# Optimization experiments

Hardware: AMD Instinct MI355X
Metric: run time of the kernel (lower is better)

The kernel has to match this reference:

```python
import jax, jax.numpy as jnp
import numpy as np


def silu(x):
    return x * jax.nn.sigmoid(x)


def conv1x1(x, w, s, b, act):
    # x: [B,Ci,H,W], w: [Co,Ci]; BN folded into per-channel scale s / bias b
    y = jnp.einsum('oi,bihw->bohw', w, x) * s[None, :, None, None] + b[None, :, None, None]
    return silu(y) if act else y


def dwconv3x3(x, w, s, b):
    # depthwise 3x3, groups=C, padding SAME (autopad=1); w: [C,1,3,3]
    y = jax.lax.conv_general_dilated(
        x, w, window_strides=(1, 1), padding=[(1, 1), (1, 1)],
        dimension_numbers=('NCHW', 'OIHW', 'NCHW'),
        feature_group_count=x.shape[1])
    return y * s[None, :, None, None] + b[None, :, None, None]


def attention(x, qkv_w, qkv_s, qkv_b, pe_w, pe_s, pe_b, proj_w, proj_s, proj_b,
              num_heads=4, key_dim=32, head_dim=64):
    B, C, H, W = x.shape
    N = H * W
    scale = key_dim ** -0.5
    qkv = conv1x1(x, qkv_w, qkv_s, qkv_b, act=False)          # [B, C+2*nh*kd, H, W]
    qkv = qkv.reshape(B, num_heads, key_dim * 2 + head_dim, N)
    q = qkv[:, :, :key_dim]                                    # [B,nh,kd,N]
    k = qkv[:, :, key_dim:2 * key_dim]                         # [B,nh,kd,N]
    v = qkv[:, :, 2 * key_dim:]                                # [B,nh,hd,N]
    attn = jnp.einsum('bhdi,bhdj->bhij', q, k) * scale         # [B,nh,N,N]
    attn = jax.nn.softmax(attn, axis=-1)
    out = jnp.einsum('bhdj,bhij->bhdi', v, attn)               # [B,nh,hd,N]
    out = out.reshape(B, C, H, W) + dwconv3x3(v.reshape(B, C, H, W), pe_w, pe_s, pe_b)
    return conv1x1(out, proj_w, proj_s, proj_b, act=False)


def setup_inputs() -> dict:
    key = jax.random.key(0)
    ks = jax.random.split(key, 32)
    B, C1, H, W = 4, 512, 48, 48
    c = C1 // 2  # 256
    h = c + 2 * 32 * 4  # 512
    d = {'x': jax.random.normal(ks[0], (B, C1, H, W), jnp.float32)}
    def w(i, shape):
        return jax.random.normal(ks[i], shape, jnp.float32) * 0.05
    def s(i, n):
        return jax.random.uniform(ks[i], (n,), jnp.float32, 0.5, 1.5)
    def b(i, n):
        return jax.random.normal(ks[i], (n,), jnp.float32) * 0.05
    d['cv1_w'], d['cv1_s'], d['cv1_b'] = w(1, (2 * c, C1)), s(2, 2 * c), b(3, 2 * c)
    d['qkv_w'], d['qkv_s'], d['qkv_b'] = w(4, (h, c)), s(5, h), b(6, h)
    d['pe_w'], d['pe_s'], d['pe_b'] = w(7, (c, 1, 3, 3)), s(8, c), b(9, c)
    d['proj_w'], d['proj_s'], d['proj_b'] = w(10, (c, c)), s(11, c), b(12, c)
    d['ffn1_w'], d['ffn1_s'], d['ffn1_b'] = w(13, (2 * c, c)), s(14, 2 * c), b(15, 2 * c)
    d['ffn2_w'], d['ffn2_s'], d['ffn2_b'] = w(16, (c, 2 * c)), s(17, c), b(18, c)
    d['cv2_w'], d['cv2_s'], d['cv2_b'] = w(19, (C1, 2 * c)), s(20, C1), b(21, C1)
    return d


def reference(x, cv1_w, cv1_s, cv1_b, qkv_w, qkv_s, qkv_b, pe_w, pe_s, pe_b,
              proj_w, proj_s, proj_b, ffn1_w, ffn1_s, ffn1_b, ffn2_w, ffn2_s, ffn2_b,
              cv2_w, cv2_s, cv2_b):
    c = cv1_w.shape[0] // 2  # hidden channels (256)
    ab = conv1x1(x, cv1_w, cv1_s, cv1_b, act=True)
    a, bb = ab[:, :c], ab[:, c:]
    bb = bb + attention(bb, qkv_w, qkv_s, qkv_b, pe_w, pe_s, pe_b,
                        proj_w, proj_s, proj_b)
    f = conv1x1(bb, ffn1_w, ffn1_s, ffn1_b, act=True)
    bb = bb + conv1x1(f, ffn2_w, ffn2_s, ffn2_b, act=False)
    return conv1x1(jnp.concatenate([a, bb], axis=1), cv2_w, cv2_s, cv2_b, act=True)
```

## Files before the change

kernel.cpp:

```cpp
#include <hip/hip_runtime.h>
#include <math.h>

#define N_SP 2304
#define HW 48

typedef unsigned short u16;
typedef short s8v  __attribute__((ext_vector_type(8)));
typedef short s4v  __attribute__((ext_vector_type(4)));
typedef u16   u16x8 __attribute__((ext_vector_type(8)));
typedef float f32x4 __attribute__((ext_vector_type(4)));
typedef unsigned u32x4 __attribute__((ext_vector_type(4)));

__device__ __forceinline__ short f2bf(float x) {
    unsigned u = __float_as_uint(x);
    u += 0x7FFFu + ((u >> 16) & 1u);
    return (short)(u >> 16);
}
__device__ __forceinline__ float bf2f(u16 u) {
    return __uint_as_float((unsigned)u << 16);
}
__device__ __forceinline__ float fexp2(float x) { return __builtin_amdgcn_exp2f(x); }
__device__ __forceinline__ float frcp(float x)  { return __builtin_amdgcn_rcpf(x); }
__device__ __forceinline__ float fsilu(float v) {
    return v * frcp(1.f + fexp2(-1.4426950408889634f * v));
}
__device__ __forceinline__ unsigned cvtpk(float lo, float hi) {
    unsigned r;
    asm("v_cvt_pk_bf16_f32 %0, %1, %2" : "=v"(r) : "v"(lo), "v"(hi));
    return r;
}
__device__ __forceinline__ void gload16(const void* g, void* l) {
    __builtin_amdgcn_global_load_lds(
        (const __attribute__((address_space(1))) void*)g,
        (__attribute__((address_space(3))) void*)l, 16, 0, 0);
}
__device__ __forceinline__ void bar_lgkm() {
    asm volatile("s_waitcnt lgkmcnt(0)" ::: "memory");
    __builtin_amdgcn_s_barrier();
}

__global__ __launch_bounds__(256) void prep(
    const float* __restrict__ X, u16* __restrict__ XT,
    const float* __restrict__ s0, const float* __restrict__ s1,
    const float* __restrict__ s2, const float* __restrict__ s3,
    const float* __restrict__ s4, const float* __restrict__ s5,
    u16* __restrict__ d0, u16* __restrict__ d1, u16* __restrict__ d2,
    u16* __restrict__ d3, u16* __restrict__ d4, u16* __restrict__ d5)
{
    __shared__ float tile[64][65];
    const int t = threadIdx.x;
    if (blockIdx.x < 960) {
        int id = blockIdx.x * 256 + t;
        const int c0 = 65536, c1 = c0 + 32768, c2 = c1 + 16384,
                  c3 = c2 + 32768, c4 = c3 + 32768, c5 = c4 + 65536;
        if (id >= c5) return;
        const float* s; u16* d; int off;
        if      (id < c0) { s = s0; d = d0; off = id; }
        else if (id < c1) { s = s1; d = d1; off = id - c0; }
        else if (id < c2) { s = s2; d = d2; off = id - c1; }
        else if (id < c3) { s = s3; d = d3; off = id - c2; }
        else if (id < c4) { s = s4; d = d4; off = id - c3; }
        else              { s = s5; d = d5; off = id - c4; }
        float4 v = ((const float4*)s)[off];
        s4v p; p[0] = f2bf(v.x); p[1] = f2bf(v.y); p[2] = f2bf(v.z); p[3] = f2bf(v.w);
        ((s4v*)d)[off] = p;
        return;
    }
    const int bid = blockIdx.x - 960;
    const int n0 = (bid % 36) * 64, c0 = ((bid / 36) & 7) * 64, b = bid / 288;
    const float* src = X + (long)b * 512 * N_SP;
    u16* dst = XT + (long)b * N_SP * 512;
    #pragma unroll
    for (int it = 0; it < 16; ++it) {
        int id = t + 256 * it;
        int cl = id >> 6, nl = id & 63;
        tile[cl][nl] = src[(long)(c0 + cl) * N_SP + n0 + nl];
    }
    __syncthreads();
    #pragma unroll
    for (int it = 0; it < 16; ++it) {
        int id = t + 256 * it;
        int nl = id >> 6, cl = id & 63;
        dst[(long)(n0 + nl) * 512 + c0 + cl] = f2bf(tile[cl][nl]);
    }
}

template <int NO, int OMODE>
__global__ __launch_bounds__(256) void mfma_gemm(
    const u16* __restrict__ A1, const u16* __restrict__ A2, int K1,
    int sA1, int sA2, int K,
    const u16* __restrict__ W,
    const float* __restrict__ S, const float* __restrict__ Bi,
    const u16* __restrict__ Res, int sR,
    void* __restrict__ OutP, u16* __restrict__ OutT, int sO, int Mtot,
    int act)
{
    __shared__ u16 Al[3][64][64];
    __shared__ u16 Bl[3][64][64];
    const int t  = threadIdx.x;
    const int p = blockIdx.x;
    const int cx = p & 7, q = p >> 3;
    const int n0 = (cx * 18 + q / NO) * 64;
    const int o0 = (q % NO) * 64;
    const int lane = t & 63, w = t >> 6;
    const int wn = (w & 1) * 32, wo = (w >> 1) * 32;
    const int li = lane & 15, g = lane >> 4;

    const int b_blk = n0 / N_SP;
    const int n_in0 = n0 - b_blk * N_SP;

    f32x4 acc[2][2];
    #pragma unroll
    for (int fm = 0; fm < 2; ++fm)
        #pragma unroll
        for (int fn = 0; fn < 2; ++fn) acc[fm][fn] = f32x4{0.f, 0.f, 0.f, 0.f};

    auto issue = [&](int buf, int k0) {
        #pragma unroll
        for (int qq = 0; qq < 2; ++qq) {
            int c = t + qq * 256;
            int row = c >> 3;
            int col = ((c & 7) ^ (row & 7)) * 8;
            int kk = k0 + col;
            const u16* ga = (kk < K1) ? (A1 + (long)(n0 + row) * sA1 + kk)
                                      : (A2 + (long)(n0 + row) * sA2 + (kk - K1));
            gload16(ga, (u16*)Al[buf] + (qq * 256 + w * 64) * 8);
            gload16(W + (long)(o0 + row) * K + k0 + col,
                    (u16*)Bl[buf] + (qq * 256 + w * 64) * 8);
        }
    };

    const int NK = K >> 6;
    issue(0, 0);
    if (NK > 1) issue(1, 64);

    for (int ks = 0; ks < NK; ++ks) {
        if (ks + 1 < NK) asm volatile("s_waitcnt vmcnt(4)" ::: "memory");
        else             asm volatile("s_waitcnt vmcnt(0)" ::: "memory");
        __builtin_amdgcn_s_barrier();
        if (ks + 2 < NK) issue((ks + 2) % 3, (ks + 2) << 6);
        const int cur = ks % 3;
        #pragma unroll
        for (int k2 = 0; k2 < 2; ++k2) {
            s8v af[2], bfv[2];
            #pragma unroll
            for (int fm = 0; fm < 2; ++fm) {
                int row = wn + fm * 16 + li;
                af[fm] = *(const s8v*)&Al[cur][row][((g + 4 * k2) ^ (li & 7)) * 8];
            }
            #pragma unroll
            for (int fn = 0; fn < 2; ++fn) {
                int row = wo + fn * 16 + li;
                bfv[fn] = *(const s8v*)&Bl[cur][row][((g + 4 * k2) ^ (li & 7)) * 8];
            }
            #pragma unroll
            for (int fm = 0; fm < 2; ++fm)
                #pragma unroll
                for (int fn = 0; fn < 2; ++fn)
                    acc[fm][fn] = __builtin_amdgcn_mfma_f32_16x16x32_bf16(
                        af[fm], bfv[fn], acc[fm][fn], 0, 0, 0);
        }
    }

    #pragma unroll
    for (int fn = 0; fn < 2; ++fn) {
        const int o = o0 + wo + fn * 16 + li;
        const float sc2 = S[o], bi = Bi[o];
        #pragma unroll
        for (int fm = 0; fm < 2; ++fm) {
            const int nb  = n0 + wn + fm * 16 + 4 * g;
            const int nib = n_in0 + wn + fm * 16 + 4 * g;
            float y[4];
            #pragma unroll
            for (int r = 0; r < 4; ++r) {
                float v = acc[fm][fn][r] * sc2 + bi;
                if (act) v = fsilu(v);
                y[r] = v;
            }
            if (Res) {
                #pragma unroll
                for (int r = 0; r < 4; ++r)
                    y[r] += bf2f(Res[(long)(nb + r) * sR + o]);
            }
            if (OMODE == 0) {
                u16* O = (u16*)OutP;
                #pragma unroll
                for (int r = 0; r < 4; ++r)
                    O[(long)(nb + r) * sO + o] = (u16)f2bf(y[r]);
            } else if (OMODE == 1 || OMODE == 3) {
                u16* O = (u16*)OutP + (long)b_blk * Mtot * N_SP + (long)o * N_SP + nib;
                s4v pk;
                #pragma unroll
                for (int r = 0; r < 4; ++r) pk[r] = f2bf(y[r]);
                *(s4v*)O = pk;
                if (OMODE == 3) {
                    #pragma unroll
                    for (int r = 0; r < 4; ++r)
                        OutT[(long)(nb + r) * 512 + o] = (u16)f2bf(y[r]);
                }
            } else {
                float* O = (float*)OutP + (long)b_blk * Mtot * N_SP + (long)o * N_SP + nib;
                *(float4*)O = make_float4(y[0], y[1], y[2], y[3]);
            }
        }
    }
}

__global__ __launch_bounds__(256) void attn_mfma(const u16* __restrict__ qkv,
    const u16* __restrict__ qkvT,
    u16* __restrict__ Opart, float* __restrict__ mpart, float* __restrict__ lpart)
{
    const int N = N_SP;
    __shared__ u16 Klds[2][64][40];
    __shared__ u16 Vlds[2][64][72];

    const int p = blockIdx.x;
    const int cx = p & 7, q = p >> 3;
    const int i0 = (q % 18) * 128;
    const int bhz = cx + 8 * (q / 18);
    const int bh = bhz & 15, z = bhz >> 4;
    const int b = bh >> 2, h = bh & 3;
    const int t = threadIdx.x;
    const int w = t >> 6;
    const int lane = t & 63;
    const int li = lane & 15;
    const int g  = lane >> 4;
    const float qscale = 0.17677669529663687f * 1.4426950408889634f;

    const u16* qp  = qkv  + ((long)b * 512 + (long)h * 128) * N;
    const u16* vp  = qp + 64L * N;
    const u16* qTp = qkvT + (long)b * N * 512 + h * 128;

    const int ia = i0 + w * 16 + li;
    const int ib = ia + 64;

    s8v qf[2];
    {
        s8v qa = *(const s8v*)(qTp + (long)ia * 512 + 8 * g);
        s8v qb = *(const s8v*)(qTp + (long)ib * 512 + 8 * g);
        #pragma unroll
        for (int r = 0; r < 8; ++r) {
            qf[0][r] = f2bf(bf2f((u16)qa[r]) * qscale);
            qf[1][r] = f2bf(bf2f((u16)qb[r]) * qscale);
        }
    }

    f32x4 oacc[2][4];
    #pragma unroll
    for (int q2 = 0; q2 < 2; ++q2)
        #pragma unroll
        for (int dt = 0; dt < 4; ++dt) oacc[q2][dt] = f32x4{0.f, 0.f, 0.f, 0.f};
    float m_run[2] = {-1e30f, -1e30f}, l_run[2] = {0.f, 0.f};

    const int kj2 = t & 63;
    const int kd  = (t >> 6) * 8;
    const int vd  = t >> 2;
    const int vjb = (t & 3) * 16;

    const int jbase = z * 576;
    u16x8 kr, vr0, vr1;
    auto ldregs = [&](int j0) {
        kr  = *(const u16x8*)(qTp + (long)(j0 + kj2) * 512 + 32 + kd);
        vr0 = *(const u16x8*)(vp + (long)vd * N + j0 + vjb);
        vr1 = *(const u16x8*)(vp + (long)vd * N + j0 + vjb + 8);
    };

    ldregs(jbase);
    *(u16x8*)&Klds[0][kj2][kd]     = kr;
    *(u16x8*)&Vlds[0][vd][vjb]     = vr0;
    *(u16x8*)&Vlds[0][vd][vjb + 8] = vr1;
    ldregs(jbase + 64);
    bar_lgkm();

    int cur = 0;
    for (int it = 0; it < 9; ++it) {
        if (it + 1 < 9) {
            *(u16x8*)&Klds[cur ^ 1][kj2][kd]     = kr;
            *(u16x8*)&Vlds[cur ^ 1][vd][vjb]     = vr0;
            *(u16x8*)&Vlds[cur ^ 1][vd][vjb + 8] = vr1;
            if (it + 2 < 9) ldregs(jbase + (it + 2) * 64);
        }

        f32x4 sacc[2][4];
        __builtin_amdgcn_s_setprio(1);
        #pragma unroll
        for (int js = 0; js < 4; ++js) {
            s8v kf = *(const s8v*)&Klds[cur][js * 16 + li][8 * g];
            f32x4 zz = f32x4{0.f, 0.f, 0.f, 0.f};
            sacc[0][js] = __builtin_amdgcn_mfma_f32_16x16x32_bf16(kf, qf[0], zz, 0, 0, 0);
            sacc[1][js] = __builtin_amdgcn_mfma_f32_16x16x32_bf16(kf, qf[1], zz, 0, 0, 0);
        }
        __builtin_amdgcn_s_setprio(0);

        #pragma unroll
        for (int q2 = 0; q2 < 2; ++q2) {
            float tm = -1e30f;
            #pragma unroll
            for (int js = 0; js < 4; ++js)
                #pragma unroll
                for (int r = 0; r < 4; ++r) tm = fmaxf(tm, sacc[q2][js][r]);
            tm = fmaxf(tm, __shfl_xor(tm, 16, 64));
            tm = fmaxf(tm, __shfl_xor(tm, 32, 64));
            if (__any(tm > m_run[q2] + 8.f)) {
                float mnew = fmaxf(m_run[q2], tm);
                float scl  = fexp2(m_run[q2] - mnew);
                l_run[q2] *= scl;
                #pragma unroll
                for (int dt = 0; dt < 4; ++dt) oacc[q2][dt] *= scl;
                m_run[q2] = mnew;
            }
            float ts = 0.f;
            #pragma unroll
            for (int js = 0; js < 4; ++js)
                #pragma unroll
                for (int r = 0; r < 4; ++r) {
                    float pv = fexp2(sacc[q2][js][r] - m_run[q2]);
                    sacc[q2][js][r] = pv;
                    ts += pv;
                }
            ts += __shfl_xor(ts, 16, 64);
            ts += __shfl_xor(ts, 32, 64);
            l_run[q2] += ts;
        }

        __builtin_amdgcn_s_setprio(1);
        #pragma unroll
        for (int ks = 0; ks < 2; ++ks) {
            s8v pf[2];
            #pragma unroll
            for (int q2 = 0; q2 < 2; ++q2) {
                u32x4 pw;
                pw[0] = cvtpk(sacc[q2][2 * ks][0],     sacc[q2][2 * ks][1]);
                pw[1] = cvtpk(sacc[q2][2 * ks][2],     sacc[q2][2 * ks][3]);
                pw[2] = cvtpk(sacc[q2][2 * ks + 1][0], sacc[q2][2 * ks + 1][1]);
                pw[3] = cvtpk(sacc[q2][2 * ks + 1][2], sacc[q2][2 * ks + 1][3]);
                pf[q2] = __builtin_bit_cast(s8v, pw);
            }
            #pragma unroll
            for (int dt = 0; dt < 4; ++dt) {
                int d = dt * 16 + li;
                s4v lo = *(const s4v*)&Vlds[cur][d][32 * ks + 4 * g];
                s4v hi = *(const s4v*)&Vlds[cur][d][32 * ks + 16 + 4 * g];
                s8v vf = __builtin_shufflevector(lo, hi, 0, 1, 2, 3, 4, 5, 6, 7);
                oacc[0][dt] = __builtin_amdgcn_mfma_f32_16x16x32_bf16(vf, pf[0], oacc[0][dt], 0, 0, 0);
                oacc[1][dt] = __builtin_amdgcn_mfma_f32_16x16x32_bf16(vf, pf[1], oacc[1][dt], 0, 0, 0);
            }
        }
        __builtin_amdgcn_s_setprio(0);

        if (it + 1 < 9) bar_lgkm();
        cur ^= 1;
    }

    const long cb = (long)(z * 16 + bh);
    #pragma unroll
    for (int q2 = 0; q2 < 2; ++q2) {
        const int i = q2 ? ib : ia;
        #pragma unroll
        for (int dt = 0; dt < 4; ++dt)
            #pragma unroll
            for (int r = 0; r < 4; ++r)
                Opart[(cb * 64 + dt * 16 + 4 * g + r) * N + i] = (u16)f2bf(oacc[q2][dt][r]);
        if (g == 0) {
            mpart[cb * N + i] = m_run[q2];
            lpart[cb * N + i] = l_run[q2];
        }
    }
}

__global__ __launch_bounds__(256) void attn_combine(
    const u16* __restrict__ Opart, const float* __restrict__ mpart,
    const float* __restrict__ lpart, const u16* __restrict__ qkvT,
    const float* __restrict__ pw, const float* __restrict__ ps,
    const float* __restrict__ pb, u16* __restrict__ attnT)
{
    const int N = N_SP;
    const int i0 = blockIdx.x * 64;
    const int bh = blockIdx.y;
    const int b = bh >> 2, h = bh & 3;
    const int t = threadIdx.x;
    const int il = t & 63, dq = t >> 6;
    const int d0 = dq * 16;
    const int i = i0 + il;

    float mm[4], ll[4];
    #pragma unroll
    for (int c = 0; c < 4; ++c) {
        mm[c] = mpart[((long)(c * 16 + bh)) * N + i];
        ll[c] = lpart[((long)(c * 16 + bh)) * N + i];
    }
    float ms = fmaxf(fmaxf(mm[0], mm[1]), fmaxf(mm[2], mm[3]));
    float wc[4], lsum = 0.f;
    #pragma unroll
    for (int c = 0; c < 4; ++c) {
        wc[c] = fexp2(mm[c] - ms);
        lsum += wc[c] * ll[c];
    }
    float inv = frcp(lsum);

    const int y = i / HW, x = i - (i / HW) * HW;
    const u16* vT = qkvT + (long)b * N * 512 + h * 128 + 64 + d0;
    float pe[16];
    #pragma unroll
    for (int dd = 0; dd < 16; ++dd) pe[dd] = 0.f;
    #pragma unroll
    for (int dy = -1; dy <= 1; ++dy) {
        int yy = y + dy;
        if (yy < 0 || yy >= HW) continue;
        #pragma unroll
        for (int dx = -1; dx <= 1; ++dx) {
            int xx = x + dx;
            if (xx < 0 || xx >= HW) continue;
            const int k = (dy + 1) * 3 + (dx + 1);
            const u16* pvt = vT + (long)(yy * HW + xx) * 512;
            u16x8 a0 = *(const u16x8*)pvt;
            u16x8 a1 = *(const u16x8*)(pvt + 8);
            #pragma unroll
            for (int dd = 0; dd < 8; ++dd) {
                pe[dd]     += pw[(h * 64 + d0 + dd) * 9 + k]     * bf2f((u16)a0[dd]);
                pe[8 + dd] += pw[(h * 64 + d0 + 8 + dd) * 9 + k] * bf2f((u16)a1[dd]);
            }
        }
    }

    u16 ob[16];
    #pragma unroll
    for (int dd = 0; dd < 16; ++dd) {
        const int d = d0 + dd;
        const int cg = h * 64 + d;
        float o = 0.f;
        #pragma unroll
        for (int c = 0; c < 4; ++c)
            o += wc[c] * bf2f(Opart[((long)(c * 16 + bh) * 64 + d) * N + i]);
        o = o * inv + pe[dd] * ps[cg] + pb[cg];
        ob[dd] = (u16)f2bf(o);
    }
    u16* dst = attnT + ((long)b * N + i) * 256 + h * 64 + d0;
    *(u16x8*)dst       = *(u16x8*)&ob[0];
    *(u16x8*)(dst + 8) = *(u16x8*)&ob[8];
}

extern "C" void kernel_launch(void* const* d_in, const int* in_sizes, int n_in,
                              void* d_out, int out_size, void* d_ws, size_t ws_size,
                              hipStream_t stream)
{
    const long N = N_SP;
    const float* x      = (const float*)d_in[0];
    const float* cv1_w  = (const float*)d_in[1];
    const float* cv1_s  = (const float*)d_in[2];
    const float* cv1_b  = (const float*)d_in[3];
    const float* qkv_w  = (const float*)d_in[4];
    const float* qkv_s  = (const float*)d_in[5];
    const float* qkv_b  = (const float*)d_in[6];
    const float* pe_w   = (const float*)d_in[7];
    const float* pe_s   = (const float*)d_in[8];
    const float* pe_b   = (const float*)d_in[9];
    const float* proj_w = (const float*)d_in[10];
    const float* proj_s = (const float*)d_in[11];
    const float* proj_b = (const float*)d_in[12];
    const float* ffn1_w = (const float*)d_in[13];
    const float* ffn1_s = (const float*)d_in[14];
    const float* ffn1_b = (const float*)d_in[15];
    const float* ffn2_w = (const float*)d_in[16];
    const float* ffn2_s = (const float*)d_in[17];
    const float* ffn2_b = (const float*)d_in[18];
    const float* cv2_w  = (const float*)d_in[19];
    const float* cv2_s  = (const float*)d_in[20];
    const float* cv2_b  = (const float*)d_in[21];
    float* out = (float*)d_out;

    u16* ws = (u16*)d_ws;
    u16* xT      = ws;
    u16* abT     = xT      + 4L * N * 512;
    u16* qkvb    = abT     + 4L * N * 512;
    u16* qkvT    = qkvb    + 4L * N * 512;
    u16* attnT   = qkvT    + 4L * N * 512;
    u16* bb2T    = attnT   + 4L * N * 256;
    u16* fT      = bb2T    + 4L * N * 256;
    u16* bb3T    = fT      + 4L * N * 512;
    u16* w_cv1   = bb3T    + 4L * N * 256;
    u16* w_qkv   = w_cv1   + 512L * 512;
    u16* w_proj  = w_qkv   + 512L * 256;
    u16* w_ffn1  = w_proj  + 256L * 256;
    u16* w_ffn2  = w_ffn1  + 512L * 256;
    u16* w_cv2   = w_ffn2  + 256L * 512;
    u16* Opart   = w_cv2   + 512L * 512;
    float* mpart = (float*)(Opart + 4L * 16 * 64 * N);
    float* lpart = mpart + 4L * 16 * N;

    dim3 blk(256);
    const int BIGK = 1 << 28;

    prep<<<2112, blk, 0, stream>>>(x, xT,
        cv1_w, qkv_w, proj_w, ffn1_w, ffn2_w, cv2_w,
        w_cv1, w_qkv, w_proj, w_ffn1, w_ffn2, w_cv2);

    mfma_gemm<8, 0><<<1152, blk, 0, stream>>>(
        xT, nullptr, BIGK, 512, 0, 512, w_cv1, cv1_s, cv1_b,
        nullptr, 0, abT, nullptr, 512, 512, 1);

    mfma_gemm<8, 3><<<1152, blk, 0, stream>>>(
        abT + 256, nullptr, BIGK, 512, 0, 256, w_qkv, qkv_s, qkv_b,
        nullptr, 0, qkvb, qkvT, 0, 512, 0);

    attn_mfma<<<1152, blk, 0, stream>>>(qkvb, qkvT, Opart, mpart, lpart);

    attn_combine<<<dim3(36, 16), blk, 0, stream>>>(
        Opart, mpart, lpart, qkvT, pe_w, pe_s, pe_b, attnT);

    mfma_gemm<4, 0><<<576, blk, 0, stream>>>(
        attnT, nullptr, BIGK, 256, 0, 256, w_proj, proj_s, proj_b,
        abT + 256, 512, bb2T, nullptr, 256, 256, 0);

    mfma_gemm<8, 0><<<1152, blk, 0, stream>>>(
        bb2T, nullptr, BIGK, 256, 0, 256, w_ffn1, ffn1_s, ffn1_b,
        nullptr, 0, fT, nullptr, 512, 512, 1);

    mfma_gemm<4, 0><<<576, blk, 0, stream>>>(
        fT, nullptr, BIGK, 512, 0, 512, w_ffn2, ffn2_s, ffn2_b,
        bb2T, 256, bb3T, nullptr, 256, 256, 0);

    mfma_gemm<8, 2><<<1152, blk, 0, stream>>>(
        abT, bb3T, 256, 512, 256, 512, w_cv2, cv2_s, cv2_b,
        nullptr, 0, out, nullptr, 0, 512, 1);
}
```

Measured before the change: 129.7 us.

## Add 128x64 tile GEMM variant and use it for the wide 1x1 convs

Adds a new MFMA GEMM kernel with a 128-row spatial by 64-channel output tile and double-buffered LDS, replacing the triple-buffered 64x64 variant. It is used for the four GEMMs with 512 output channels, halving their grid to 576 blocks. The epilogue is factored into a shared helper. Larger tiles raise operand reuse per LDS load and cut redundant weight and activation fetches, in exchange for more accumulator registers, fewer blocks (possibly lower occupancy on 256 CUs), and a shallower prefetch pipeline.

```diff
diff --git a/kernel.cpp b/kernel.cpp
--- a/kernel.cpp
+++ b/kernel.cpp
@@ -85,6 +85,38 @@
     }
 }
 
+template <int OMODE>
+__device__ __forceinline__ void gemm_epilogue(
+    float y[4], int nb, int nib, int o, int b_blk, int Mtot,
+    const u16* Res, int sR, void* OutP, u16* OutT, int sO)
+{
+    if (Res) {
+        #pragma unroll
+        for (int r = 0; r < 4; ++r)
+            y[r] += bf2f(Res[(long)(nb + r) * sR + o]);
+    }
+    if (OMODE == 0) {
+        u16* O = (u16*)OutP;
+        #pragma unroll
+        for (int r = 0; r < 4; ++r)
+            O[(long)(nb + r) * sO + o] = (u16)f2bf(y[r]);
+    } else if (OMODE == 1 || OMODE == 3) {
+        u16* O = (u16*)OutP + (long)b_blk * Mtot * N_SP + (long)o * N_SP + nib;
+        s4v pk;
+        #pragma unroll
+        for (int r = 0; r < 4; ++r) pk[r] = f2bf(y[r]);
+        *(s4v*)O = pk;
+        if (OMODE == 3) {
+            #pragma unroll
+            for (int r = 0; r < 4; ++r)
+                OutT[(long)(nb + r) * 512 + o] = (u16)f2bf(y[r]);
+        }
+    } else {
+        float* O = (float*)OutP + (long)b_blk * Mtot * N_SP + (long)o * N_SP + nib;
+        *(float4*)O = make_float4(y[0], y[1], y[2], y[3]);
+    }
+}
+
 template <int NO, int OMODE>
 __global__ __launch_bounds__(256) void mfma_gemm(
     const u16* __restrict__ A1, const u16* __restrict__ A2, int K1,
@@ -177,31 +209,113 @@
                 if (act) v = fsilu(v);
                 y[r] = v;
             }
-            if (Res) {
+            gemm_epilogue<OMODE>(y, nb, nib, o, b_blk, Mtot, Res, sR, OutP, OutT, sO);
+        }
+    }
+}
+
+template <int NO, int OMODE>
+__global__ __launch_bounds__(256) void mfma_gemm_big(
+    const u16* __restrict__ A1, const u16* __restrict__ A2, int K1,
+    int sA1, int sA2, int K,
+    const u16* __restrict__ W,
+    const float* __restrict__ S, const float* __restrict__ Bi,
+    const u16* __restrict__ Res, int sR,
+    void* __restrict__ OutP, u16* __restrict__ OutT, int sO, int Mtot,
+    int act)
+{
+    __shared__ u16 Al[2][128][64];
+    __shared__ u16 Bl[2][64][64];
+    const int t  = threadIdx.x;
+    const int p = blockIdx.x;
+    const int cx = p & 7, q = p >> 3;
+    const int n0 = (cx * 9 + q / NO) * 128;
+    const int o0 = (q % NO) * 64;
+    const int lane = t & 63, w = t >> 6;
+    const int wn = (w & 1) * 64, wo = (w >> 1) * 32;
+    const int li = lane & 15, g = lane >> 4;
+
+    const int b_blk = n0 / N_SP;
+    const int n_in0 = n0 - b_blk * N_SP;
+
+    f32x4 acc[4][2];
+    #pragma unroll
+    for (int fm = 0; fm < 4; ++fm)
+        #pragma unroll
+        for (int fn = 0; fn < 2; ++fn) acc[fm][fn] = f32x4{0.f, 0.f, 0.f, 0.f};
+
+    auto issue = [&](int buf, int k0) {
+        #pragma unroll
+        for (int qq = 0; qq < 4; ++qq) {
+            int c = t + qq * 256;
+            int row = c >> 3;
+            int col = ((c & 7) ^ (row & 7)) * 8;
+            int kk = k0 + col;
+            const u16* ga = (kk < K1) ? (A1 + (long)(n0 + row) * sA1 + kk)
+                                      : (A2 + (long)(n0 + row) * sA2 + (kk - K1));
+            gload16(ga, (u16*)Al[buf] + (qq * 256 + w * 64) * 8);
+        }
+        #pragma unroll
+        for (int qq = 0; qq < 2; ++qq) {
+            int c = t + qq * 256;
+            int row = c >> 3;
+            int col = ((c & 7) ^ (row & 7)) * 8;
+            gload16(W + (long)(o0 + row) * K + k0 + col,
+                    (u16*)Bl[buf] + (qq * 256 + w * 64) * 8);
+        }
+    };
+
+    const int NK = K >> 6;
+    issue(0, 0);
+    asm volatile("s_waitcnt vmcnt(0)" ::: "memory");
+    __builtin_amdgcn_s_barrier();
+
+    int cur = 0;
+    for (int ks = 0; ks < NK; ++ks) {
+        if (ks + 1 < NK) issue(cur ^ 1, (ks + 1) << 6);
+        #pragma unroll
+        for (int k2 = 0; k2 < 2; ++k2) {
+            s8v af[4], bfv[2];
+            #pragma unroll
+            for (int fm = 0; fm < 4; ++fm) {
+                int row = wn + fm * 16 + li;
+                af[fm] = *(const s8v*)&Al[cur][row][((g + 4 * k2) ^ (li & 7)) * 8];
+            }
+            #pragma unroll
+            for (int fn = 0; fn < 2; ++fn) {
+                int row = wo + fn * 16 + li;
+                bfv[fn] = *(const s8v*)&Bl[cur][row][((g + 4 * k2) ^ (li & 7)) * 8];
+            }
+            #pragma unroll
+            for (int fm = 0; fm < 4; ++fm)
                 #pragma unroll
-                for (int r = 0; r < 4; ++r)
-                    y[r] += bf2f(Res[(long)(nb + r) * sR + o]);
-            }
-            if (OMODE == 0) {
-                u16* O = (u16*)OutP;
-                #pragma unroll
-                for (int r = 0; r < 4; ++r)
-                    O[(long)(nb + r) * sO + o] = (u16)f2bf(y[r]);
-            } else if (OMODE == 1 || OMODE == 3) {
-                u16* O = (u16*)OutP + (long)b_blk * Mtot * N_SP + (long)o * N_SP + nib;
-                s4v pk;
-                #pragma unroll
-                for (int r = 0; r < 4; ++r) pk[r] = f2bf(y[r]);
-                *(s4v*)O = pk;
-                if (OMODE == 3) {
-                    #pragma unroll
-                    for (int r = 0; r < 4; ++r)
-                        OutT[(long)(nb + r) * 512 + o] = (u16)f2bf(y[r]);
-                }
-            } else {
-                float* O = (float*)OutP + (long)b_blk * Mtot * N_SP + (long)o * N_SP + nib;
-                *(float4*)O = make_float4(y[0], y[1], y[2], y[3]);
-            }
+                for (int fn = 0; fn < 2; ++fn)
+                    acc[fm][fn] = __builtin_amdgcn_mfma_f32_16x16x32_bf16(
+                        af[fm], bfv[fn], acc[fm][fn], 0, 0, 0);
+        }
+        if (ks + 1 < NK) {
+            asm volatile("s_waitcnt vmcnt(0)" ::: "memory");
+            __builtin_amdgcn_s_barrier();
+        }
+        cur ^= 1;
+    }
+
+    #pragma unroll
+    for (int fn = 0; fn < 2; ++fn) {
+        const int o = o0 + wo + fn * 16 + li;
+        const float sc2 = S[o], bi = Bi[o];
+        #pragma unroll
+        for (int fm = 0; fm < 4; ++fm) {
+            const int nb  = n0 + wn + fm * 16 + 4 * g;
+            const int nib = n_in0 + wn + fm * 16 + 4 * g;
+            float y[4];
+            #pragma unroll
+            for (int r = 0; r < 4; ++r) {
+                float v = acc[fm][fn][r] * sc2 + bi;
+                if (act) v = fsilu(v);
+                y[r] = v;
+            }
+            gemm_epilogue<OMODE>(y, nb, nib, o, b_blk, Mtot, Res, sR, OutP, OutT, sO);
         }
     }
 }
@@ -495,11 +609,11 @@
         cv1_w, qkv_w, proj_w, ffn1_w, ffn2_w, cv2_w,
         w_cv1, w_qkv, w_proj, w_ffn1, w_ffn2, w_cv2);
 
-    mfma_gemm<8, 0><<<1152, blk, 0, stream>>>(
+    mfma_gemm_big<8, 0><<<576, blk, 0, stream>>>(
         xT, nullptr, BIGK, 512, 0, 512, w_cv1, cv1_s, cv1_b,
         nullptr, 0, abT, nullptr, 512, 512, 1);
 
-    mfma_gemm<8, 3><<<1152, blk, 0, stream>>>(
+    mfma_gemm_big<8, 3><<<576, blk, 0, stream>>>(
         abT + 256, nullptr, BIGK, 512, 0, 256, w_qkv, qkv_s, qkv_b,
         nullptr, 0, qkvb, qkvT, 0, 512, 0);
 
@@ -512,7 +626,7 @@
         attnT, nullptr, BIGK, 256, 0, 256, w_proj, proj_s, proj_b,
         abT + 256, 512, bb2T, nullptr, 256, 256, 0);
 
-    mfma_gemm<8, 0><<<1152, blk, 0, stream>>>(
+    mfma_gemm_big<8, 0><<<576, blk, 0, stream>>>(
         bb2T, nullptr, BIGK, 256, 0, 256, w_ffn1, ffn1_s, ffn1_b,
         nullptr, 0, fT, nullptr, 512, 512, 1);
 
@@ -520,7 +634,7 @@
         fT, nullptr, BIGK, 512, 0, 512, w_ffn2, ffn2_s, ffn2_b,
         bb2T, 256, bb3T, nullptr, 256, 256, 0);
 
-    mfma_gemm<8, 2><<<1152, blk, 0, stream>>>(
+    mfma_gemm_big<8, 2><<<576, blk, 0, stream>>>(
         abT, bb3T, 256, 512, 256, 512, w_cv2, cv2_s, cv2_b,
         nullptr, 0, out, nullptr, 0, 512, 1);
 }
```

New measurement: 125.6 us, median of 2. -3.2%, faster.
